# Kernel optimization log

Hardware: AMD Instinct MI355X
Metric: run time of the kernel (lower is better)

Reference implementation:

```python
import jax, jax.numpy as jnp
import numpy as np

CO, NO, ITERATIONS, STRIDE = 32, 8, 3, 2


def _squash(x, axis):
    norm = jnp.linalg.norm(x, axis=axis, keepdims=True)
    return x * norm / (1.0 + norm ** 2)


def _quantize(x, bits):
    # Faithful instantiation: identity quantization (full-precision pass-through),
    # matching running the original module with quantization_function = lambda t, b: t.
    return x


def setup_inputs() -> dict:
    key = jax.random.key(0)
    k1, k2, k3 = jax.random.split(key, 3)
    x = jax.random.normal(k1, (16, 256, 1, 20, 20), dtype=jnp.float32)
    W = jax.random.normal(k2, (CO * NO, 1, 9, 9), dtype=jnp.float32) * 0.05  # Conv2d weight [co*no, ni, k, k]
    bias = jax.random.normal(k3, (CO, NO, 1, 1), dtype=jnp.float32) * 0.01
    return {"x": x, "W": W, "bias": bias,
            "quantization_bits": 8, "quantization_bits_routing": 8}


def reference(x, W, bias, quantization_bits, quantization_bits_routing):
    bs, ci, ni, hi, wi = x.shape
    # vote generation: conv over each input capsule channel independently
    lhs = x.reshape(bs * ci, ni, hi, wi)
    votes = jax.lax.conv_general_dilated(
        lhs, W, window_strides=(STRIDE, STRIDE), padding='VALID',
        dimension_numbers=('NCHW', 'OIHW', 'NCHW'))
    votes = _quantize(votes, quantization_bits)
    ho, wo = votes.shape[-2:]
    votes = votes.reshape(bs, ci, CO, NO, ho, wo)  # [bs, ci, co, no, ho, wo]

    logits = jnp.zeros((bs, ci, CO, ho, wo), dtype=votes.dtype)
    activation = None
    for _ in range(ITERATIONS):
        route = jax.nn.softmax(logits, axis=2)                      # c_ij over co
        route = _quantize(route, quantization_bits)
        # s_j = sum_i c_ij * u_hat_{j|i} + bias  -> [bs, co, no, ho, wo]
        preactivate = jnp.einsum('bichw,bicnhw->bcnhw', route, votes) + bias
        preactivate = _quantize(preactivate, quantization_bits_routing)
        activation = _squash(preactivate, axis=2)                   # squash over no
        activation = _quantize(activation, quantization_bits)
        # agreement: <u_hat_{j|i}, v_j> summed over no -> [bs, ci, co, ho, wo]
        distances = jnp.einsum('bicnhw,bcnhw->bichw', votes, activation)
        logits = _quantize(logits + distances, quantization_bits_routing)
    return activation
```

## Files before the change

kernel.cpp:

```cpp
#include <hip/hip_runtime.h>


#define BS 16
#define CI 256
#define CO 32
#define NO 8
#define HI 20
#define WI 20
#define HO 6
#define WO 6
#define NPIX 36
#define NTAP 81
#define XP 104
#define NBLK 256

typedef __attribute__((ext_vector_type(8))) short bf16x8;
typedef __attribute__((ext_vector_type(4))) float f32x4;

__device__ __forceinline__ ushort f2bf(float x) {
    union { float f; unsigned u; } v; v.f = x;
    unsigned r = v.u + 0x7FFFu + ((v.u >> 16) & 1u);
    return (ushort)(r >> 16);
}

template<int CTRL>
__device__ __forceinline__ float dpp_radd(float v) {
    int s = __builtin_amdgcn_update_dpp(0, __float_as_int(v), CTRL, 0xF, 0xF, true);
    return v + __int_as_float(s);
}
__device__ __forceinline__ float row16_sum_tail(float v) {
    v = dpp_radd<0x111>(v);
    v = dpp_radd<0x112>(v);
    v = dpp_radd<0x114>(v);
    v = dpp_radd<0x118>(v);
    return v;
}
__device__ __forceinline__ float grp8_sum_all(float v) {
    v = dpp_radd<0xB1>(v);
    v = dpp_radd<0x4E>(v);
    v = dpp_radd<0x141>(v);
    return v;
}
#if __has_builtin(__builtin_amdgcn_permlane16_swap)
typedef unsigned u32x2 __attribute__((ext_vector_type(2)));
__device__ __forceinline__ float xor16_sum(float v) {
    u32x2 r = __builtin_amdgcn_permlane16_swap(__float_as_uint(v), __float_as_uint(v), false, false);
    return __uint_as_float(r.x) + __uint_as_float(r.y);
}
#else
__device__ __forceinline__ float xor16_sum(float v) { return v + __shfl_xor(v, 16, 64); }
#endif
#if __has_builtin(__builtin_amdgcn_permlane32_swap)
typedef unsigned u32x2b __attribute__((ext_vector_type(2)));
__device__ __forceinline__ float xor32_sum(float v) {
    u32x2b r = __builtin_amdgcn_permlane32_swap(__float_as_uint(v), __float_as_uint(v), false, false);
    return __uint_as_float(r.x) + __uint_as_float(r.y);
}
#else
__device__ __forceinline__ float xor32_sum(float v) { return v + __shfl_xor(v, 32, 64); }
#endif

#if __has_builtin(__builtin_amdgcn_exp2f)
#define EXPFN(x) __builtin_amdgcn_exp2f(x)
#define ASCALE 1.44269504f
#else
#define EXPFN(x) __expf(x)
#define ASCALE 1.0f
#endif

__device__ __forceinline__ void stage_x(const float* __restrict__ xb,
                                        ushort* __restrict__ xw,
                                        int t, int h, int w) {
    const int w2 = 2 * w;
    #pragma unroll 1
    for (int idx = t; idx < CI * 9 * 4; idx += 1024) {
        int q4 = idx & 3, r = idx >> 2;
        int kh = r % 9, i = r / 9;
        float4 v = *(const float4*)(xb + (i * HI + 2 * h + kh) * WI + 4 * q4);
        const float* ve = &v.x;
        #pragma unroll
        for (int e = 0; e < 4; ++e) {
            int kw = 4 * q4 + e - w2;
            if ((unsigned)kw < 9u) xw[i * XP + kh * 9 + kw] = f2bf(ve[e]);
        }
    }
    if (w >= 4) {
        #pragma unroll 1
        for (int r = t; r < CI * 9; r += 1024) {
            int kh = r % 9, i = r / 9;
            float4 v = *(const float4*)(xb + (i * HI + 2 * h + kh) * WI + 16);
            const float* ve = &v.x;
            #pragma unroll
            for (int e = 0; e < 4; ++e) {
                int kw = 16 + e - w2;
                if ((unsigned)kw < 9u) xw[i * XP + kh * 9 + kw] = f2bf(ve[e]);
            }
        }
    }
}

__global__ __launch_bounds__(1024) void caps_kernel(
    const float* __restrict__ x,
    const float* __restrict__ Wt,
    const float* __restrict__ bias,
    float* __restrict__ out)
{
    __shared__ __align__(16) ushort xw[CI * XP];
    __shared__ __align__(16) ushort wl[CO * NO * XP];
    __shared__ __align__(16) float  smx[4 * 256];
    __shared__ __align__(16) float  pre[4 * 256];
    __shared__ __align__(16) float  act[256];

    const int t   = threadIdx.x, blk = blockIdx.x;
    const int b   = blk & 15;
    const int npix = (blk < 64) ? 3 : 2;
    const float* xb = x + b * CI * HI * WI;

    const int wid = t >> 6, l = t & 63;
    const int q = l >> 4, il = l & 15;
    const int wf = wid >> 2, wi = wid & 3;

    {
        const int f = t >> 2, c4 = t & 3, k0 = c4 * 20;
        const float* ws = Wt + f * NTAP + k0;
        ushort* wd = wl + f * XP + k0;
        #pragma unroll
        for (int j = 0; j < 20; ++j) wd[j] = f2bf(ws[j]);
        if (c4 == 3) wd[20] = f2bf(ws[20]);
    }
    {
        int i = t >> 2, s4 = t & 3;
        #pragma unroll
        for (int j = 0; j < 6; ++j) {
            int k = NTAP + s4 * 6 + j;
            if (k < XP) { xw[i * XP + k] = 0; wl[i * XP + k] = 0; }
        }
    }
    stage_x(xb, xw, t, (blk >> 4) / WO, (blk >> 4) % WO);

    const float bias_r = (t < 256) ? bias[t] : 0.f;

    for (int p = 0; p < npix; ++p) {
        const int hw = (blk + 256 * p) >> 4;

        __syncthreads();

        f32x4 acc[4][4];
        #pragma unroll
        for (int tf = 0; tf < 4; ++tf)
            #pragma unroll
            for (int ti = 0; ti < 4; ++ti)
                acc[tf][ti] = (f32x4){0.f, 0.f, 0.f, 0.f};

        #pragma unroll
        for (int ks = 0; ks < 3; ++ks) {
            const int ko = ks * 32 + q * 8;
            bf16x8 af[4], bv[4];
            #pragma unroll
            for (int tf = 0; tf < 4; ++tf)
                af[tf] = *(const bf16x8*)&wl[(wf * 64 + tf * 16 + il) * XP + ko];
            #pragma unroll
            for (int ti = 0; ti < 4; ++ti)
                bv[ti] = *(const bf16x8*)&xw[(wi * 64 + ti * 16 + il) * XP + ko];
            #pragma unroll
            for (int tf = 0; tf < 4; ++tf)
                #pragma unroll
                for (int ti = 0; ti < 4; ++ti)
                    acc[tf][ti] = __builtin_amdgcn_mfma_f32_16x16x32_bf16(
                        af[tf], bv[ti], acc[tf][ti], 0, 0, 0);
        }

        __syncthreads();

        if (p + 1 < npix) {
            const int hwn = (blk + 256 * (p + 1)) >> 4;
            stage_x(xb, xw, t, hwn / WO, hwn % WO);
        }

        float lg[4][4];
        #pragma unroll
        for (int tf = 0; tf < 4; ++tf)
            #pragma unroll
            for (int ti = 0; ti < 4; ++ti) lg[tf][ti] = 0.f;

        #pragma unroll
        for (int it = 0; it < 3; ++it) {
            float pp[4][4];
            if (it == 0) {
                #pragma unroll
                for (int tf = 0; tf < 4; ++tf)
                    #pragma unroll
                    for (int r = 0; r < 4; ++r)
                        pp[tf][r] = (acc[tf][0][r] + acc[tf][1][r]
                                   + acc[tf][2][r] + acc[tf][3][r]) * 0.03125f;
            } else {
                float e[4][4], srow[4] = {0.f, 0.f, 0.f, 0.f};
                #pragma unroll
                for (int tf = 0; tf < 4; ++tf)
                    #pragma unroll
                    for (int ti = 0; ti < 4; ++ti) {
                        e[tf][ti] = EXPFN(lg[tf][ti]);
                        srow[ti] += e[tf][ti];
                    }
                #pragma unroll
                for (int ti = 0; ti < 4; ++ti)
                    srow[ti] = xor32_sum(srow[ti]);
                if (q == 0) {
                    #pragma unroll
                    for (int ti = 0; ti < 4; ++ti)
                        smx[wf * 256 + wi * 64 + ti * 16 + il] = srow[ti];
                }
                __syncthreads();
                float rtot[4];
                #pragma unroll
                for (int ti = 0; ti < 4; ++ti) {
                    int i = wi * 64 + ti * 16 + il;
                    rtot[ti] = __builtin_amdgcn_rcpf(
                        smx[i] + smx[256 + i] + smx[512 + i] + smx[768 + i]);
                }
                float route[4][4];
                #pragma unroll
                for (int tf = 0; tf < 4; ++tf)
                    #pragma unroll
                    for (int ti = 0; ti < 4; ++ti) route[tf][ti] = e[tf][ti] * rtot[ti];
                #pragma unroll
                for (int tf = 0; tf < 4; ++tf)
                    #pragma unroll
                    for (int r = 0; r < 4; ++r)
                        pp[tf][r] = route[tf][0] * acc[tf][0][r] + route[tf][1] * acc[tf][1][r]
                                  + route[tf][2] * acc[tf][2][r] + route[tf][3] * acc[tf][3][r];
            }

            #pragma unroll
            for (int tf = 0; tf < 4; ++tf)
                #pragma unroll
                for (int r = 0; r < 4; ++r)
                    pp[tf][r] = row16_sum_tail(pp[tf][r]);
            if (il == 15) {
                #pragma unroll
                for (int tf = 0; tf < 4; ++tf) {
                    int c = wf * 8 + tf * 2 + (q >> 1);
                    f32x4 vv = {pp[tf][0], pp[tf][1], pp[tf][2], pp[tf][3]};
                    *(f32x4*)&pre[wi * 256 + c * 8 + (q & 1) * 4] = vv;
                }
            }
            __syncthreads();

            if (t < 256) {
                float s = bias_r + pre[t] + pre[256 + t] + pre[512 + t] + pre[768 + t];
                float sq = grp8_sum_all(s * s);
                float a = s * __builtin_amdgcn_sqrtf(sq) * __builtin_amdgcn_rcpf(1.f + sq);
                if (it == 2) {
                    int c = t >> 3, n = t & 7;
                    out[((b * CO + c) * NO + n) * NPIX + hw] = a;
                } else {
                    act[t] = a * ASCALE;
                }
            }

            if (it < 2) {
                __syncthreads();
                #pragma unroll
                for (int tf = 0; tf < 4; ++tf) {
                    int c = wf * 8 + tf * 2 + (q >> 1);
                    f32x4 av = *(const f32x4*)&act[c * 8 + (q & 1) * 4];
                    #pragma unroll
                    for (int ti = 0; ti < 4; ++ti) {
                        float d = acc[tf][ti][0] * av[0] + acc[tf][ti][1] * av[1]
                                + acc[tf][ti][2] * av[2] + acc[tf][ti][3] * av[3];
                        lg[tf][ti] += xor16_sum(d);
                    }
                }
            }
        }
    }
}

extern "C" void kernel_launch(void* const* d_in, const int* in_sizes, int n_in,
                              void* d_out, int out_size, void* d_ws, size_t ws_size,
                              hipStream_t stream) {
    const float* x    = (const float*)d_in[0];
    const float* Wt   = (const float*)d_in[1];
    const float* bias = (const float*)d_in[2];
    float* out = (float*)d_out;
    caps_kernel<<<NBLK, 1024, 0, stream>>>(x, Wt, bias, out);
}
```

Measured before the change: 46.12 us.

## Give each wave all output filters for 16 input capsules to localize softmax

```diff
diff --git a/kernel.cpp b/kernel.cpp
--- a/kernel.cpp
+++ b/kernel.cpp
@@ -107,8 +107,7 @@
 {
     __shared__ __align__(16) ushort xw[CI * XP];
     __shared__ __align__(16) ushort wl[CO * NO * XP];
-    __shared__ __align__(16) float  smx[4 * 256];
-    __shared__ __align__(16) float  pre[4 * 256];
+    __shared__ __align__(16) float  pre[16 * 256];
     __shared__ __align__(16) float  act[256];
 
     const int t   = threadIdx.x, blk = blockIdx.x;
@@ -118,7 +117,6 @@
 
     const int wid = t >> 6, l = t & 63;
     const int q = l >> 4, il = l & 15;
-    const int wf = wid >> 2, wi = wid & 3;
 
     {
         const int f = t >> 2, c4 = t & 3, k0 = c4 * 20;
@@ -145,29 +143,20 @@
 
         __syncthreads();
 
-        f32x4 acc[4][4];
-        #pragma unroll
-        for (int tf = 0; tf < 4; ++tf)
-            #pragma unroll
-            for (int ti = 0; ti < 4; ++ti)
-                acc[tf][ti] = (f32x4){0.f, 0.f, 0.f, 0.f};
+        f32x4 acc[16];
+        #pragma unroll
+        for (int tile = 0; tile < 16; ++tile)
+            acc[tile] = (f32x4){0.f, 0.f, 0.f, 0.f};
 
         #pragma unroll
         for (int ks = 0; ks < 3; ++ks) {
             const int ko = ks * 32 + q * 8;
-            bf16x8 af[4], bv[4];
+            bf16x8 bv = *(const bf16x8*)&xw[(wid * 16 + il) * XP + ko];
             #pragma unroll
-            for (int tf = 0; tf < 4; ++tf)
-                af[tf] = *(const bf16x8*)&wl[(wf * 64 + tf * 16 + il) * XP + ko];
-            #pragma unroll
-            for (int ti = 0; ti < 4; ++ti)
-                bv[ti] = *(const bf16x8*)&xw[(wi * 64 + ti * 16 + il) * XP + ko];
-            #pragma unroll
-            for (int tf = 0; tf < 4; ++tf)
-                #pragma unroll
-                for (int ti = 0; ti < 4; ++ti)
-                    acc[tf][ti] = __builtin_amdgcn_mfma_f32_16x16x32_bf16(
-                        af[tf], bv[ti], acc[tf][ti], 0, 0, 0);
+            for (int tile = 0; tile < 16; ++tile) {
+                bf16x8 af = *(const bf16x8*)&wl[(tile * 16 + il) * XP + ko];
+                acc[tile] = __builtin_amdgcn_mfma_f32_16x16x32_bf16(af, bv, acc[tile], 0, 0, 0);
+            }
         }
 
         __syncthreads();
@@ -177,77 +166,35 @@
             stage_x(xb, xw, t, hwn / WO, hwn % WO);
         }
 
-        float lg[4][4];
-        #pragma unroll
-        for (int tf = 0; tf < 4; ++tf)
+        float lg[16];
+        #pragma unroll
+        for (int tile = 0; tile < 16; ++tile) lg[tile] = 0.f;
+
+        #pragma unroll
+        for (int it = 0; it < 3; ++it) {
+            float rtot = 0.03125f;
+            if (it > 0) {
+                float den = 0.f;
+                #pragma unroll
+                for (int tile = 0; tile < 16; ++tile) den += EXPFN(lg[tile]);
+                rtot = __builtin_amdgcn_rcpf(xor32_sum(den));
+            }
+
             #pragma unroll
-            for (int ti = 0; ti < 4; ++ti) lg[tf][ti] = 0.f;
-
-        #pragma unroll
-        for (int it = 0; it < 3; ++it) {
-            float pp[4][4];
-            if (it == 0) {
-                #pragma unroll
-                for (int tf = 0; tf < 4; ++tf)
-                    #pragma unroll
-                    for (int r = 0; r < 4; ++r)
-                        pp[tf][r] = (acc[tf][0][r] + acc[tf][1][r]
-                                   + acc[tf][2][r] + acc[tf][3][r]) * 0.03125f;
-            } else {
-                float e[4][4], srow[4] = {0.f, 0.f, 0.f, 0.f};
-                #pragma unroll
-                for (int tf = 0; tf < 4; ++tf)
-                    #pragma unroll
-                    for (int ti = 0; ti < 4; ++ti) {
-                        e[tf][ti] = EXPFN(lg[tf][ti]);
-                        srow[ti] += e[tf][ti];
-                    }
-                #pragma unroll
-                for (int ti = 0; ti < 4; ++ti)
-                    srow[ti] = xor32_sum(srow[ti]);
-                if (q == 0) {
-                    #pragma unroll
-                    for (int ti = 0; ti < 4; ++ti)
-                        smx[wf * 256 + wi * 64 + ti * 16 + il] = srow[ti];
-                }
-                __syncthreads();
-                float rtot[4];
-                #pragma unroll
-                for (int ti = 0; ti < 4; ++ti) {
-                    int i = wi * 64 + ti * 16 + il;
-                    rtot[ti] = __builtin_amdgcn_rcpf(
-                        smx[i] + smx[256 + i] + smx[512 + i] + smx[768 + i]);
-                }
-                float route[4][4];
-                #pragma unroll
-                for (int tf = 0; tf < 4; ++tf)
-                    #pragma unroll
-                    for (int ti = 0; ti < 4; ++ti) route[tf][ti] = e[tf][ti] * rtot[ti];
-                #pragma unroll
-                for (int tf = 0; tf < 4; ++tf)
-                    #pragma unroll
-                    for (int r = 0; r < 4; ++r)
-                        pp[tf][r] = route[tf][0] * acc[tf][0][r] + route[tf][1] * acc[tf][1][r]
-                                  + route[tf][2] * acc[tf][2][r] + route[tf][3] * acc[tf][3][r];
-            }
-
-            #pragma unroll
-            for (int tf = 0; tf < 4; ++tf)
-                #pragma unroll
-                for (int r = 0; r < 4; ++r)
-                    pp[tf][r] = row16_sum_tail(pp[tf][r]);
-            if (il == 15) {
-                #pragma unroll
-                for (int tf = 0; tf < 4; ++tf) {
-                    int c = wf * 8 + tf * 2 + (q >> 1);
-                    f32x4 vv = {pp[tf][0], pp[tf][1], pp[tf][2], pp[tf][3]};
-                    *(f32x4*)&pre[wi * 256 + c * 8 + (q & 1) * 4] = vv;
-                }
+            for (int tile = 0; tile < 16; ++tile) {
+                const float rt = (it == 0) ? rtot : EXPFN(lg[tile]) * rtot;
+                f32x4 pp = acc[tile] * rt;
+                #pragma unroll
+                for (int r = 0; r < 4; ++r) pp[r] = row16_sum_tail(pp[r]);
+                if (il == 15)
+                    *(f32x4*)&pre[wid * 256 + (tile * 2 + (q >> 1)) * 8 + (q & 1) * 4] = pp;
             }
             __syncthreads();
 
             if (t < 256) {
-                float s = bias_r + pre[t] + pre[256 + t] + pre[512 + t] + pre[768 + t];
+                float s = bias_r;
+                #pragma unroll
+                for (int wv = 0; wv < 16; ++wv) s += pre[wv * 256 + t];
                 float sq = grp8_sum_all(s * s);
                 float a = s * __builtin_amdgcn_sqrtf(sq) * __builtin_amdgcn_rcpf(1.f + sq);
                 if (it == 2) {
@@ -261,15 +208,11 @@
             if (it < 2) {
                 __syncthreads();
                 #pragma unroll
-                for (int tf = 0; tf < 4; ++tf) {
-                    int c = wf * 8 + tf * 2 + (q >> 1);
-                    f32x4 av = *(const f32x4*)&act[c * 8 + (q & 1) * 4];
-                    #pragma unroll
-                    for (int ti = 0; ti < 4; ++ti) {
-                        float d = acc[tf][ti][0] * av[0] + acc[tf][ti][1] * av[1]
-                                + acc[tf][ti][2] * av[2] + acc[tf][ti][3] * av[3];
-                        lg[tf][ti] += xor16_sum(d);
-                    }
+                for (int tile = 0; tile < 16; ++tile) {
+                    f32x4 av = *(const f32x4*)&act[(tile * 2 + (q >> 1)) * 8 + (q & 1) * 4];
+                    float d = acc[tile][0] * av[0] + acc[tile][1] * av[1]
+                            + acc[tile][2] * av[2] + acc[tile][3] * av[3];
+                    lg[tile] += xor16_sum(d);
                 }
             }
         }
```

Measured after the change: 62.27 us. 35.0% more time.

## Compute first routing iteration from column-summed input patches via linearity

Applied to the files above, without the earlier changes.

```diff
diff --git a/kernel.cpp b/kernel.cpp
--- a/kernel.cpp
+++ b/kernel.cpp
@@ -22,6 +22,9 @@
     unsigned r = v.u + 0x7FFFu + ((v.u >> 16) & 1u);
     return (ushort)(r >> 16);
 }
+__device__ __forceinline__ float bf2f(short u) {
+    return __uint_as_float(((unsigned)(ushort)u) << 16);
+}
 
 template<int CTRL>
 __device__ __forceinline__ float dpp_radd(float v) {
@@ -39,6 +42,11 @@
     v = dpp_radd<0xB1>(v);
     v = dpp_radd<0x4E>(v);
     v = dpp_radd<0x141>(v);
+    return v;
+}
+__device__ __forceinline__ float quad_sum_all(float v) {
+    v = dpp_radd<0xB1>(v);
+    v = dpp_radd<0x4E>(v);
     return v;
 }
 #if __has_builtin(__builtin_amdgcn_permlane16_swap)
@@ -97,6 +105,18 @@
             }
         }
     }
+}
+
+__device__ __forceinline__ void compute_csum(const ushort* __restrict__ xw,
+                                             float* __restrict__ csum, int tt) {
+    const int k = tt >> 2, part = tt & 3;
+    const ushort* col = xw + (part * 64) * XP + k;
+    float s = 0.f;
+    #pragma unroll 4
+    for (int j = 0; j < 64; ++j)
+        s += bf2f((short)col[j * XP]);
+    s = quad_sum_all(s);
+    if (part == 0) csum[k] = s;
 }
 
 __global__ __launch_bounds__(1024) void caps_kernel(
@@ -110,6 +130,7 @@
     __shared__ __align__(16) float  smx[4 * 256];
     __shared__ __align__(16) float  pre[4 * 256];
     __shared__ __align__(16) float  act[256];
+    __shared__ __align__(16) float  csum[96];
 
     const int t   = threadIdx.x, blk = blockIdx.x;
     const int b   = blk & 15;
@@ -137,6 +158,8 @@
         }
     }
     stage_x(xb, xw, t, (blk >> 4) / WO, (blk >> 4) % WO);
+    __syncthreads();
+    if (t < 384) compute_csum(xw, csum, t);
 
     const float bias_r = (t < 256) ? bias[t] : 0.f;
 
@@ -170,6 +193,25 @@
                         af[tf], bv[ti], acc[tf][ti], 0, 0, 0);
         }
 
+        if (t < 256) {
+            const ushort* wrow = wl + t * XP;
+            float s0 = 0.f;
+            #pragma unroll 2
+            for (int kb = 0; kb < 12; ++kb) {
+                bf16x8 wv = *(const bf16x8*)&wrow[kb * 8];
+                f32x4 c0 = *(const f32x4*)&csum[kb * 8];
+                f32x4 c1 = *(const f32x4*)&csum[kb * 8 + 4];
+                s0 += bf2f(wv[0]) * c0[0] + bf2f(wv[1]) * c0[1]
+                    + bf2f(wv[2]) * c0[2] + bf2f(wv[3]) * c0[3]
+                    + bf2f(wv[4]) * c1[0] + bf2f(wv[5]) * c1[1]
+                    + bf2f(wv[6]) * c1[2] + bf2f(wv[7]) * c1[3];
+            }
+            float s = bias_r + 0.03125f * s0;
+            float sq = grp8_sum_all(s * s);
+            float a = s * __builtin_amdgcn_sqrtf(sq) * __builtin_amdgcn_rcpf(1.f + sq);
+            act[t] = a * ASCALE;
+        }
+
         __syncthreads();
 
         if (p + 1 < npix) {
@@ -184,51 +226,53 @@
             for (int ti = 0; ti < 4; ++ti) lg[tf][ti] = 0.f;
 
         #pragma unroll
-        for (int it = 0; it < 3; ++it) {
+        for (int it = 1; it <= 2; ++it) {
+            #pragma unroll
+            for (int tf = 0; tf < 4; ++tf) {
+                int c = wf * 8 + tf * 2 + (q >> 1);
+                f32x4 av = *(const f32x4*)&act[c * 8 + (q & 1) * 4];
+                #pragma unroll
+                for (int ti = 0; ti < 4; ++ti) {
+                    float d = acc[tf][ti][0] * av[0] + acc[tf][ti][1] * av[1]
+                            + acc[tf][ti][2] * av[2] + acc[tf][ti][3] * av[3];
+                    lg[tf][ti] += xor16_sum(d);
+                }
+            }
+
+            float e[4][4], srow[4] = {0.f, 0.f, 0.f, 0.f};
+            #pragma unroll
+            for (int tf = 0; tf < 4; ++tf)
+                #pragma unroll
+                for (int ti = 0; ti < 4; ++ti) {
+                    e[tf][ti] = EXPFN(lg[tf][ti]);
+                    srow[ti] += e[tf][ti];
+                }
+            #pragma unroll
+            for (int ti = 0; ti < 4; ++ti)
+                srow[ti] = xor32_sum(srow[ti]);
+            if (q == 0) {
+                #pragma unroll
+                for (int ti = 0; ti < 4; ++ti)
+                    smx[wf * 256 + wi * 64 + ti * 16 + il] = srow[ti];
+            }
+            __syncthreads();
+            float rtot[4];
+            #pragma unroll
+            for (int ti = 0; ti < 4; ++ti) {
+                int i = wi * 64 + ti * 16 + il;
+                rtot[ti] = __builtin_amdgcn_rcpf(
+                    smx[i] + smx[256 + i] + smx[512 + i] + smx[768 + i]);
+            }
             float pp[4][4];
-            if (it == 0) {
-                #pragma unroll
-                for (int tf = 0; tf < 4; ++tf)
-                    #pragma unroll
-                    for (int r = 0; r < 4; ++r)
-                        pp[tf][r] = (acc[tf][0][r] + acc[tf][1][r]
-                                   + acc[tf][2][r] + acc[tf][3][r]) * 0.03125f;
-            } else {
-                float e[4][4], srow[4] = {0.f, 0.f, 0.f, 0.f};
-                #pragma unroll
-                for (int tf = 0; tf < 4; ++tf)
-                    #pragma unroll
-                    for (int ti = 0; ti < 4; ++ti) {
-                        e[tf][ti] = EXPFN(lg[tf][ti]);
-                        srow[ti] += e[tf][ti];
-                    }
-                #pragma unroll
-                for (int ti = 0; ti < 4; ++ti)
-                    srow[ti] = xor32_sum(srow[ti]);
-                if (q == 0) {
-                    #pragma unroll
-                    for (int ti = 0; ti < 4; ++ti)
-                        smx[wf * 256 + wi * 64 + ti * 16 + il] = srow[ti];
-                }
-                __syncthreads();
-                float rtot[4];
-                #pragma unroll
-                for (int ti = 0; ti < 4; ++ti) {
-                    int i = wi * 64 + ti * 16 + il;
-                    rtot[ti] = __builtin_amdgcn_rcpf(
-                        smx[i] + smx[256 + i] + smx[512 + i] + smx[768 + i]);
-                }
-                float route[4][4];
-                #pragma unroll
-                for (int tf = 0; tf < 4; ++tf)
-                    #pragma unroll
-                    for (int ti = 0; ti < 4; ++ti) route[tf][ti] = e[tf][ti] * rtot[ti];
-                #pragma unroll
-                for (int tf = 0; tf < 4; ++tf)
-                    #pragma unroll
-                    for (int r = 0; r < 4; ++r)
-                        pp[tf][r] = route[tf][0] * acc[tf][0][r] + route[tf][1] * acc[tf][1][r]
-                                  + route[tf][2] * acc[tf][2][r] + route[tf][3] * acc[tf][3][r];
+            #pragma unroll
+            for (int tf = 0; tf < 4; ++tf) {
+                float route[4];
+                #pragma unroll
+                for (int ti = 0; ti < 4; ++ti) route[ti] = e[tf][ti] * rtot[ti];
+                #pragma unroll
+                for (int r = 0; r < 4; ++r)
+                    pp[tf][r] = route[0] * acc[tf][0][r] + route[1] * acc[tf][1][r]
+                              + route[2] * acc[tf][2][r] + route[3] * acc[tf][3][r];
             }
 
             #pragma unroll
@@ -257,20 +301,9 @@
                     act[t] = a * ASCALE;
                 }
             }
-
-            if (it < 2) {
+            if (it == 1) {
+                if (p + 1 < npix && t >= 640) compute_csum(xw, csum, t - 640);
                 __syncthreads();
-                #pragma unroll
-                for (int tf = 0; tf < 4; ++tf) {
-                    int c = wf * 8 + tf * 2 + (q >> 1);
-                    f32x4 av = *(const f32x4*)&act[c * 8 + (q & 1) * 4];
-                    #pragma unroll
-                    for (int ti = 0; ti < 4; ++ti) {
-                        float d = acc[tf][ti][0] * av[0] + acc[tf][ti][1] * av[1]
-                                + acc[tf][ti][2] * av[2] + acc[tf][ti][3] * av[3];
-                        lg[tf][ti] += xor16_sum(d);
-                    }
-                }
             }
         }
     }
```

New measurement: 48.02 us. +4.1%, slower.
